# Kernel optimization log

Measured on AMD Instinct MI355X. Metric: run time of the kernel, lower is better.

Reference implementation:

```python
import jax, jax.numpy as jnp
import numpy as np

NUM_HEADS = 4

def setup_inputs() -> dict:
    key = jax.random.key(0)
    ks = jax.random.split(key, 8)
    B_, N, C = 4096, 49, 128
    nW = 64
    return {
        "x": jax.random.normal(ks[0], (B_, N, C), dtype=jnp.float32),
        "mask": jax.random.normal(ks[1], (nW, N, N), dtype=jnp.float32),
        "qkv_w": jax.random.normal(ks[2], (3 * C, C), dtype=jnp.float32) * 0.02,
        "qkv_b": jax.random.normal(ks[3], (3 * C,), dtype=jnp.float32) * 0.02,
        "proj_w": jax.random.normal(ks[4], (C, C), dtype=jnp.float32) * 0.02,
        "proj_b": jax.random.normal(ks[5], (C,), dtype=jnp.float32) * 0.02,
        "rpb_table": jax.random.normal(ks[6], (169, NUM_HEADS), dtype=jnp.float32) * 0.02,
        "rel_index": jax.random.randint(ks[7], (N, N), 0, 169, dtype=jnp.int64),
    }

def reference(x, mask, qkv_w, qkv_b, proj_w, proj_b, rpb_table, rel_index):
    B_, N, C = x.shape
    H = NUM_HEADS
    hd = C // H
    scale = hd ** -0.5
    # qkv projection: [B_, N, 3, H, hd] -> (3, B_, H, N, hd)
    qkv = (x @ qkv_w.T + qkv_b).reshape(B_, N, 3, H, hd).transpose(2, 0, 3, 1, 4)
    q, k, v = qkv[0], qkv[1], qkv[2]
    q = q * scale
    attn = jnp.einsum('bhnd,bhmd->bhnm', q, k)  # [B_, H, N, N]
    # relative position bias gather: [N*N, H] -> [H, N, N]
    bias = rpb_table[rel_index.reshape(-1)].reshape(N, N, H).transpose(2, 0, 1)
    attn = attn + bias[None]
    # window mask add: view (B_//nW, nW, H, N, N) + mask[None, :, None]
    nW = mask.shape[0]
    attn = attn.reshape(B_ // nW, nW, H, N, N) + mask[None, :, None]
    attn = attn.reshape(B_, H, N, N)
    attn = jax.nn.softmax(attn, axis=-1)
    out = jnp.einsum('bhnm,bhmd->bhnd', attn, v)  # [B_, H, N, hd]
    out = out.transpose(0, 2, 1, 3).reshape(B_, N, C)
    out = out @ proj_w.T + proj_b
    return out
```

## Files before the change

### kernel.cpp

```cpp
#include <hip/hip_runtime.h>
#include <stdint.h>

typedef __attribute__((ext_vector_type(4))) float f32x4;
typedef __attribute__((ext_vector_type(2))) float f32x2;
typedef __attribute__((ext_vector_type(8))) short s16x8;
typedef __attribute__((ext_vector_type(4))) short s16x4;
typedef __attribute__((ext_vector_type(8))) __bf16 bf16x8;
typedef __attribute__((ext_vector_type(2))) __bf16 bf16x2;
typedef __attribute__((ext_vector_type(2))) unsigned u32x2;

#define SCALE 0.17677669529663687f
#define LOG2E 1.4426950408889634f

__device__ __forceinline__ unsigned f2bf(float f) {
  unsigned u = __builtin_bit_cast(unsigned, f);
  u += 0x7fffu + ((u >> 16) & 1u);
  return u >> 16;
}
__device__ __forceinline__ unsigned pk2(float lo, float hi) {
  f32x2 v; v[0] = lo; v[1] = hi;
  bf16x2 h = __builtin_convertvector(v, bf16x2);
  return __builtin_bit_cast(unsigned, h);
}
__device__ __forceinline__ unsigned short cv1(float v) {
  return (unsigned short)f2bf(v);
}

__device__ __forceinline__ f32x4 MFMA(s16x8 a, s16x8 b, f32x4 c) {
  return __builtin_amdgcn_mfma_f32_16x16x32_bf16(
      __builtin_bit_cast(bf16x8, a), __builtin_bit_cast(bf16x8, b), c, 0, 0, 0);
}
__device__ __forceinline__ f32x4 MFMA16(u32x2 a, u32x2 b, f32x4 c) {
#if __has_builtin(__builtin_amdgcn_mfma_f32_16x16x16bf16_1k)
  return __builtin_amdgcn_mfma_f32_16x16x16bf16_1k(
      __builtin_bit_cast(s16x4, a), __builtin_bit_cast(s16x4, b), c, 0, 0, 0);
#else
  f32x4 d;
  asm("v_mfma_f32_16x16x16_bf16 %0, %1, %2, %3"
      : "=v"(d) : "v"(a), "v"(b), "v"(c));
  return d;
#endif
}

template <int MODE>
__global__ __launch_bounds__(256, 4)
void win_attn(const float* __restrict__ x,
              const float* __restrict__ mask,
              const float* __restrict__ qkv_bs,
              const float* __restrict__ proj_b,
              const unsigned short* __restrict__ wq_bf,
              const unsigned short* __restrict__ wp_bf,
              const float* __restrict__ bias_full,
              const float* __restrict__ bias_pad,
              const float* __restrict__ mask_pad,
              const float* __restrict__ comb,
              float* __restrict__ out) {
  __shared__ alignas(16) char smem[16384];
  const int tid = threadIdx.x;
  const int l = tid & 63, w = tid >> 6;
  const int lr = l & 15, lq = l >> 4;
  const int b = blockIdx.x;
  const int wq = b & 63;

  {
    const float* xw = x + (size_t)b * (49 * 128);
    #pragma unroll
    for (int i = 0; i < 4; ++i) {
      const int r = w * 4 + lq + i * 16;
      s16x8 v = {};
      if (r < 49) {
        const float4* p = reinterpret_cast<const float4*>(xw + r * 128 + lr * 8);
        float4 f0 = p[0], f1 = p[1];
        union { unsigned u[4]; s16x8 v8; } U;
        U.u[0] = pk2(f0.x, f0.y); U.u[1] = pk2(f0.z, f0.w);
        U.u[2] = pk2(f1.x, f1.y); U.u[3] = pk2(f1.z, f1.w);
        v = U.v8;
      }
      *reinterpret_cast<s16x8*>(&smem[r * 256 + (((lr ^ (r & 15)) & 15) << 4)]) = v;
    }
  }
  __syncthreads();

  int addrK[4];
  #pragma unroll
  for (int kt = 0; kt < 4; ++kt)
    addrK[kt] = lr * 256 + ((((4 * kt + lq) ^ lr) & 15) << 4);

  u32x2 qB[4][2], kB[4][2], vA[2][4];
  #pragma unroll
  for (int g = 0; g < 6; ++g) {
    const int sect = g >> 1;
    const int half = g & 1;
    const int obase = sect * 128 + 32 * w + 16 * half;
    s16x8 wf[4];
    #pragma unroll
    for (int kt = 0; kt < 4; ++kt)
      wf[kt] = *reinterpret_cast<const s16x8*>(wq_bf + (obase + lr) * 128 + kt * 32 + lq * 8);
    if (sect < 2) {
      const f32x4 bia4 = *reinterpret_cast<const f32x4*>(qkv_bs + obase + 4 * lq);
      #pragma unroll
      for (int nt = 0; nt < 4; ++nt) {
        s16x8 ar[4];
        #pragma unroll
        for (int kt = 0; kt < 4; ++kt)
          ar[kt] = *reinterpret_cast<const s16x8*>(&smem[addrK[kt] + nt * 4096]);
        f32x4 acc = {};
        #pragma unroll
        for (int kt = 0; kt < 4; ++kt) acc = MFMA(wf[kt], ar[kt], acc);
        acc += bia4;
        u32x2 fr; fr[0] = pk2(acc[0], acc[1]); fr[1] = pk2(acc[2], acc[3]);
        if (sect == 0) qB[nt][half] = fr; else kB[nt][half] = fr;
      }
    } else {
      const float bo = qkv_bs[obase + lr];
      #pragma unroll
      for (int mt = 0; mt < 4; ++mt) {
        s16x8 ar[4];
        #pragma unroll
        for (int kt = 0; kt < 4; ++kt)
          ar[kt] = *reinterpret_cast<const s16x8*>(&smem[addrK[kt] + mt * 4096]);
        f32x4 acc = {};
        #pragma unroll
        for (int kt = 0; kt < 4; ++kt) acc = MFMA(ar[kt], wf[kt], acc);
        acc += bo;
        u32x2 fr; fr[0] = pk2(acc[0], acc[1]); fr[1] = pk2(acc[2], acc[3]);
        vA[half][mt] = fr;
      }
    }
  }
  __syncthreads();

  const float* biaW = bias_pad + w * 4096;
  const float* mskW = mask_pad + wq * 4096;
  const float* cW = comb + (size_t)(wq * 4 + w) * 4096;
  #pragma unroll
  for (int ntn = 0; ntn < 4; ++ntn) {
    const int n = 16 * ntn + lr;
    f32x4 add4[4];
    if (MODE == 2) {
      #pragma unroll
      for (int mtm = 0; mtm < 4; ++mtm)
        add4[mtm] = *reinterpret_cast<const f32x4*>(cW + n * 64 + 16 * mtm + 4 * lq);
    } else if (MODE == 1) {
      #pragma unroll
      for (int mtm = 0; mtm < 4; ++mtm) {
        const int m0 = 16 * mtm + 4 * lq;
        f32x4 bb = *reinterpret_cast<const f32x4*>(biaW + n * 64 + m0);
        f32x4 mm = *reinterpret_cast<const f32x4*>(mskW + n * 64 + m0);
        add4[mtm] = bb + mm;
      }
    }
    f32x4 sacc[4];
    __builtin_amdgcn_s_setprio(1);
    #pragma unroll
    for (int mtm = 0; mtm < 4; ++mtm) {
      sacc[mtm] = MFMA16(kB[mtm][0], qB[ntn][0], f32x4{});
      sacc[mtm] = MFMA16(kB[mtm][1], qB[ntn][1], sacc[mtm]);
    }
    __builtin_amdgcn_s_setprio(0);
    if (MODE >= 1) {
      #pragma unroll
      for (int mtm = 0; mtm < 4; ++mtm) sacc[mtm] += add4[mtm];
    } else {
      #pragma unroll
      for (int mtm = 0; mtm < 4; ++mtm)
        #pragma unroll
        for (int j = 0; j < 4; ++j) {
          const int m = 16 * mtm + 4 * lq + j;
          if (m < 49 && n < 49)
            sacc[mtm][j] = fmaf(bias_full[w * 2401 + n * 49 + m] + mask[wq * 2401 + n * 49 + m],
                                LOG2E, sacc[mtm][j]);
        }
    }
    {
      f32x4 v = sacc[3];
      v[0] = (lq == 0) ? v[0] : -1e30f;
      v[1] = -1e30f; v[2] = -1e30f; v[3] = -1e30f;
      sacc[3] = v;
    }
    float mx = -1e30f;
    #pragma unroll
    for (int mtm = 0; mtm < 4; ++mtm) {
      f32x4 v = sacc[mtm];
      mx = fmaxf(mx, fmaxf(fmaxf(v[0], v[1]), fmaxf(v[2], v[3])));
    }
    mx = fmaxf(mx, __shfl_xor(mx, 16, 64));
    mx = fmaxf(mx, __shfl_xor(mx, 32, 64));
    float s = 0.f;
    #pragma unroll
    for (int mtm = 0; mtm < 4; ++mtm) {
      f32x4 v = sacc[mtm];
      #pragma unroll
      for (int j = 0; j < 4; ++j) { v[j] = __builtin_exp2f(v[j] - mx); s += v[j]; }
      sacc[mtm] = v;
    }
    s += __shfl_xor(s, 16, 64);
    s += __shfl_xor(s, 32, 64);
    const float ri = 1.f / s;
    u32x2 p[4];
    #pragma unroll
    for (int mtm = 0; mtm < 4; ++mtm) {
      p[mtm][0] = pk2(sacc[mtm][0], sacc[mtm][1]);
      p[mtm][1] = pk2(sacc[mtm][2], sacc[mtm][3]);
    }
    __builtin_amdgcn_s_setprio(1);
    #pragma unroll
    for (int dt = 0; dt < 2; ++dt) {
      f32x4 oc = {};
      #pragma unroll
      for (int mtm = 0; mtm < 4; ++mtm) oc = MFMA16(vA[dt][mtm], p[mtm], oc);
      oc *= ri;
      u32x2 ov; ov[0] = pk2(oc[0], oc[1]); ov[1] = pk2(oc[2], oc[3]);
      const int cb = 64 * w + 32 * dt + 8 * lq;
      *reinterpret_cast<u32x2*>(
          &smem[n * 256 + (((((cb >> 4) ^ lr) & 15) << 4) | (cb & 15))]) = ov;
    }
    __builtin_amdgcn_s_setprio(0);
  }
  __syncthreads();

  s16x8 wpf[2][4];
  #pragma unroll
  for (int ct = 0; ct < 2; ++ct)
    #pragma unroll
    for (int kt = 0; kt < 4; ++kt)
      wpf[ct][kt] = *reinterpret_cast<const s16x8*>(
          wp_bf + (32 * w + 16 * ct + lr) * 128 + kt * 32 + lq * 8);
  float* ob = out + (size_t)b * (49 * 128);
  #pragma unroll
  for (int nt = 0; nt < 4; ++nt) {
    const int n = 16 * nt + lr;
    s16x8 osf[4];
    #pragma unroll
    for (int kt = 0; kt < 4; ++kt) {
      const int cb = 64 * kt + 16 * lq;
      osf[kt] = *reinterpret_cast<const s16x8*>(
          &smem[n * 256 + (((((cb >> 4) ^ lr) & 15) << 4) | (cb & 15))]);
    }
    #pragma unroll
    for (int ct = 0; ct < 2; ++ct) {
      const int c0 = 32 * w + 16 * ct + 4 * lq;
      f32x4 acc = {};
      #pragma unroll
      for (int kt = 0; kt < 4; ++kt) acc = MFMA(wpf[ct][kt], osf[kt], acc);
      acc += *reinterpret_cast<const f32x4*>(proj_b + c0);
      if (n < 49) *reinterpret_cast<f32x4*>(ob + n * 128 + c0) = acc;
    }
  }
}

__global__ void prep_kernel(const float* __restrict__ qkv_w,
                            const float* __restrict__ qkv_b,
                            const float* __restrict__ proj_w,
                            const float* __restrict__ rpb,
                            const int* __restrict__ rel_raw,
                            const float* __restrict__ mask,
                            unsigned short* __restrict__ wq_bf,
                            unsigned short* __restrict__ wp_bf,
                            float* __restrict__ qkv_bs,
                            float* __restrict__ bias_full,
                            float* __restrict__ bias_pad,
                            float* __restrict__ mask_pad,
                            float* __restrict__ comb,
                            int mode) {
  const int i = blockIdx.x * 256 + threadIdx.x;
  if (i < 49152) {
    float v = qkv_w[i];
    if (i < 16384) v *= SCALE * LOG2E;
    wq_bf[i] = cv1(v);
  } else if (i < 65536) {
    wp_bf[i - 49152] = cv1(proj_w[i - 49152]);
  } else if (i < 65920) {
    const int t = i - 65536;
    float v = qkv_b[t];
    if (t < 128) v *= SCALE * LOG2E;
    qkv_bs[t] = v;
  } else if (i < 75524) {
    const int t = i - 65920;
    const int h = t / 2401, nm = t % 2401;
    const bool is64 = (rel_raw[1] == 0) && (rel_raw[3] == 0) &&
                      (rel_raw[5] == 0) && (rel_raw[7] == 0);
    const int ridx = is64 ? rel_raw[2 * nm] : rel_raw[nm];
    bias_full[t] = rpb[ridx * 4 + h];
  } else if (mode == 2 && i < 75524 + 1048576) {
    const int t = i - 75524;
    const int wqi = t >> 14, h = (t >> 12) & 3, n = (t >> 6) & 63, m = t & 63;
    float v = 0.f;
    if (n < 49 && m < 49) {
      const bool is64 = (rel_raw[1] == 0) && (rel_raw[3] == 0) &&
                        (rel_raw[5] == 0) && (rel_raw[7] == 0);
      const int nm = n * 49 + m;
      const int ridx = is64 ? rel_raw[2 * nm] : rel_raw[nm];
      v = (rpb[ridx * 4 + h] + mask[wqi * 2401 + nm]) * LOG2E;
    }
    comb[t] = v;
  } else if (mode == 1 && i < 75524 + 16384) {
    const int j = i - 75524;
    const int h = j >> 12, r = (j >> 6) & 63, m = j & 63;
    float v = 0.f;
    if (r < 49 && m < 49) {
      const bool is64 = (rel_raw[1] == 0) && (rel_raw[3] == 0) &&
                        (rel_raw[5] == 0) && (rel_raw[7] == 0);
      const int nm = r * 49 + m;
      const int ridx = is64 ? rel_raw[2 * nm] : rel_raw[nm];
      v = rpb[ridx * 4 + h] * LOG2E;
    }
    bias_pad[j] = v;
  } else if (mode == 1 && i < 75524 + 16384 + 262144) {
    const int t = i - 75524 - 16384;
    const int wqi = t >> 12, n = (t >> 6) & 63, m = t & 63;
    mask_pad[t] = (n < 49 && m < 49) ? mask[wqi * 2401 + n * 49 + m] * LOG2E : 0.f;
  }
}

extern "C" void kernel_launch(void* const* d_in, const int* in_sizes, int n_in,
                              void* d_out, int out_size, void* d_ws, size_t ws_size,
                              hipStream_t stream) {
  const float* x      = (const float*)d_in[0];
  const float* mask   = (const float*)d_in[1];
  const float* qkv_w  = (const float*)d_in[2];
  const float* qkv_b  = (const float*)d_in[3];
  const float* proj_w = (const float*)d_in[4];
  const float* proj_b = (const float*)d_in[5];
  const float* rpb    = (const float*)d_in[6];
  const int*   rel    = (const int*)d_in[7];
  float* out = (float*)d_out;

  char* ws = (char*)d_ws;
  unsigned short* wq_bf = (unsigned short*)(ws + 0);
  unsigned short* wp_bf = (unsigned short*)(ws + 98304);
  float* qkv_bs    = (float*)(ws + 131072);
  float* bias_full = (float*)(ws + 132608);
  float* bias_pad  = (float*)(ws + 171024);
  float* mask_pad  = (float*)(ws + 236560);
  float* comb      = (float*)(ws + 1285376);

  int mode = 0;
  if (ws_size >= 5479680) mode = 2;
  else if (ws_size >= 1285136) mode = 1;
  const int B_ = in_sizes[0] / (49 * 128);

  const int prep_n = 75524 + (mode == 2 ? 1048576 : mode == 1 ? (16384 + 262144) : 0);
  prep_kernel<<<(prep_n + 255) / 256, 256, 0, stream>>>(
      qkv_w, qkv_b, proj_w, rpb, rel, mask,
      wq_bf, wp_bf, qkv_bs, bias_full, bias_pad, mask_pad, comb, mode);
  if (mode == 2)
    win_attn<2><<<B_, 256, 0, stream>>>(x, mask, qkv_bs, proj_b, wq_bf, wp_bf,
                                        bias_full, bias_pad, mask_pad, comb, out);
  else if (mode == 1)
    win_attn<1><<<B_, 256, 0, stream>>>(x, mask, qkv_bs, proj_b, wq_bf, wp_bf,
                                        bias_full, bias_pad, mask_pad, comb, out);
  else
    win_attn<0><<<B_, 256, 0, stream>>>(x, mask, qkv_bs, proj_b, wq_bf, wp_bf,
                                        bias_full, bias_pad, mask_pad, comb, out);
}
```

Before: 125.6 us.

## Swizzle windows across XCDs, prefetch QKV weights, drop softmax max pass

After: 131.3 us. 4.6% more time.

```diff
diff --git a/kernel.cpp b/kernel.cpp
--- a/kernel.cpp
+++ b/kernel.cpp
@@ -54,12 +54,17 @@
               const float* __restrict__ bias_pad,
               const float* __restrict__ mask_pad,
               const float* __restrict__ comb,
-              float* __restrict__ out) {
+              float* __restrict__ out,
+              int do_swz) {
   __shared__ alignas(16) char smem[16384];
   const int tid = threadIdx.x;
   const int l = tid & 63, w = tid >> 6;
   const int lr = l & 15, lq = l >> 4;
-  const int b = blockIdx.x;
+  int b = blockIdx.x;
+  if (do_swz) {
+    const int xcd = b & 7, g3 = (b >> 3) & 7, inst = b >> 6;
+    b = inst * 64 + xcd * 8 + g3;
+  }
   const int wq = b & 63;
 
   {
@@ -87,15 +92,22 @@
     addrK[kt] = lr * 256 + ((((4 * kt + lq) ^ lr) & 15) << 4);
 
   u32x2 qB[4][2], kB[4][2], vA[2][4];
+  s16x8 wf[4];
+  #pragma unroll
+  for (int kt = 0; kt < 4; ++kt)
+    wf[kt] = *reinterpret_cast<const s16x8*>(wq_bf + (32 * w + lr) * 128 + kt * 32 + lq * 8);
   #pragma unroll
   for (int g = 0; g < 6; ++g) {
     const int sect = g >> 1;
     const int half = g & 1;
     const int obase = sect * 128 + 32 * w + 16 * half;
-    s16x8 wf[4];
-    #pragma unroll
-    for (int kt = 0; kt < 4; ++kt)
-      wf[kt] = *reinterpret_cast<const s16x8*>(wq_bf + (obase + lr) * 128 + kt * 32 + lq * 8);
+    s16x8 wfn[4];
+    if (g < 5) {
+      const int obn = ((g + 1) >> 1) * 128 + 32 * w + 16 * ((g + 1) & 1);
+      #pragma unroll
+      for (int kt = 0; kt < 4; ++kt)
+        wfn[kt] = *reinterpret_cast<const s16x8*>(wq_bf + (obn + lr) * 128 + kt * 32 + lq * 8);
+    }
     if (sect < 2) {
       const f32x4 bia4 = *reinterpret_cast<const f32x4*>(qkv_bs + obase + 4 * lq);
       #pragma unroll
@@ -127,6 +139,10 @@
         vA[half][mt] = fr;
       }
     }
+    if (g < 5) {
+      #pragma unroll
+      for (int kt = 0; kt < 4; ++kt) wf[kt] = wfn[kt];
+    }
   }
   __syncthreads();
 
@@ -178,54 +194,54 @@
       v[1] = -1e30f; v[2] = -1e30f; v[3] = -1e30f;
       sacc[3] = v;
     }
-    float mx = -1e30f;
+    float s = 0.f;
     #pragma unroll
     for (int mtm = 0; mtm < 4; ++mtm) {
       f32x4 v = sacc[mtm];
-      mx = fmaxf(mx, fmaxf(fmaxf(v[0], v[1]), fmaxf(v[2], v[3])));
-    }
-    mx = fmaxf(mx, __shfl_xor(mx, 16, 64));
-    mx = fmaxf(mx, __shfl_xor(mx, 32, 64));
-    float s = 0.f;
-    #pragma unroll
-    for (int mtm = 0; mtm < 4; ++mtm) {
-      f32x4 v = sacc[mtm];
-      #pragma unroll
-      for (int j = 0; j < 4; ++j) { v[j] = __builtin_exp2f(v[j] - mx); s += v[j]; }
+      #pragma unroll
+      for (int j = 0; j < 4; ++j) { v[j] = __builtin_exp2f(v[j]); s += v[j]; }
       sacc[mtm] = v;
     }
-    s += __shfl_xor(s, 16, 64);
-    s += __shfl_xor(s, 32, 64);
-    const float ri = 1.f / s;
     u32x2 p[4];
     #pragma unroll
     for (int mtm = 0; mtm < 4; ++mtm) {
       p[mtm][0] = pk2(sacc[mtm][0], sacc[mtm][1]);
       p[mtm][1] = pk2(sacc[mtm][2], sacc[mtm][3]);
     }
+    s += __shfl_xor(s, 16, 64);
+    s += __shfl_xor(s, 32, 64);
     __builtin_amdgcn_s_setprio(1);
+    f32x4 oc[2];
     #pragma unroll
     for (int dt = 0; dt < 2; ++dt) {
-      f32x4 oc = {};
-      #pragma unroll
-      for (int mtm = 0; mtm < 4; ++mtm) oc = MFMA16(vA[dt][mtm], p[mtm], oc);
-      oc *= ri;
-      u32x2 ov; ov[0] = pk2(oc[0], oc[1]); ov[1] = pk2(oc[2], oc[3]);
+      oc[dt] = f32x4{};
+      #pragma unroll
+      for (int mtm = 0; mtm < 4; ++mtm) oc[dt] = MFMA16(vA[dt][mtm], p[mtm], oc[dt]);
+    }
+    __builtin_amdgcn_s_setprio(0);
+    const float ri = 1.f / s;
+    #pragma unroll
+    for (int dt = 0; dt < 2; ++dt) {
+      f32x4 o = oc[dt] * ri;
+      u32x2 ov; ov[0] = pk2(o[0], o[1]); ov[1] = pk2(o[2], o[3]);
       const int cb = 64 * w + 32 * dt + 8 * lq;
       *reinterpret_cast<u32x2*>(
           &smem[n * 256 + (((((cb >> 4) ^ lr) & 15) << 4) | (cb & 15))]) = ov;
     }
-    __builtin_amdgcn_s_setprio(0);
-  }
-  __syncthreads();
+  }
 
   s16x8 wpf[2][4];
-  #pragma unroll
-  for (int ct = 0; ct < 2; ++ct)
+  f32x4 pb4[2];
+  #pragma unroll
+  for (int ct = 0; ct < 2; ++ct) {
     #pragma unroll
     for (int kt = 0; kt < 4; ++kt)
       wpf[ct][kt] = *reinterpret_cast<const s16x8*>(
           wp_bf + (32 * w + 16 * ct + lr) * 128 + kt * 32 + lq * 8);
+    pb4[ct] = *reinterpret_cast<const f32x4*>(proj_b + 32 * w + 16 * ct + 4 * lq);
+  }
+  __syncthreads();
+
   float* ob = out + (size_t)b * (49 * 128);
   #pragma unroll
   for (int nt = 0; nt < 4; ++nt) {
@@ -243,7 +259,7 @@
       f32x4 acc = {};
       #pragma unroll
       for (int kt = 0; kt < 4; ++kt) acc = MFMA(wpf[ct][kt], osf[kt], acc);
-      acc += *reinterpret_cast<const f32x4*>(proj_b + c0);
+      acc += pb4[ct];
       if (n < 49) *reinterpret_cast<f32x4*>(ob + n * 128 + c0) = acc;
     }
   }
@@ -339,6 +355,7 @@
   if (ws_size >= 5479680) mode = 2;
   else if (ws_size >= 1285136) mode = 1;
   const int B_ = in_sizes[0] / (49 * 128);
+  const int do_swz = (B_ % 64 == 0) ? 1 : 0;
 
   const int prep_n = 75524 + (mode == 2 ? 1048576 : mode == 1 ? (16384 + 262144) : 0);
   prep_kernel<<<(prep_n + 255) / 256, 256, 0, stream>>>(
@@ -346,11 +363,11 @@
       wq_bf, wp_bf, qkv_bs, bias_full, bias_pad, mask_pad, comb, mode);
   if (mode == 2)
     win_attn<2><<<B_, 256, 0, stream>>>(x, mask, qkv_bs, proj_b, wq_bf, wp_bf,
-                                        bias_full, bias_pad, mask_pad, comb, out);
+                                        bias_full, bias_pad, mask_pad, comb, out, do_swz);
   else if (mode == 1)
     win_attn<1><<<B_, 256, 0, stream>>>(x, mask, qkv_bs, proj_b, wq_bf, wp_bf,
-                                        bias_full, bias_pad, mask_pad, comb, out);
+                                        bias_full, bias_pad, mask_pad, comb, out, do_swz);
   else
     win_attn<0><<<B_, 256, 0, stream>>>(x, mask, qkv_bs, proj_b, wq_bf, wp_bf,
-                                        bias_full, bias_pad, mask_pad, comb, out);
-}
+                                        bias_full, bias_pad, mask_pad, comb, out, do_swz);
+}
```
